# Kernel tuning notes

Measured on AMD Instinct MI355X. Metric: run time of the kernel, lower is better.

## Reference

```python
import jax, jax.numpy as jnp
import numpy as np

D_MODEL = 1024
NUM_HEADS = 16
D_K = D_MODEL // NUM_HEADS


def setup_inputs() -> dict:
    key = jax.random.key(0)
    ks = jax.random.split(key, 11)
    s = 1.0 / np.sqrt(D_MODEL)
    return {
        "Q": jax.random.normal(ks[0], (2, 2048, D_MODEL), jnp.float32),
        "K": jax.random.normal(ks[1], (2, 2048, D_MODEL), jnp.float32),
        "V": jax.random.normal(ks[2], (2, 2048, D_MODEL), jnp.float32),
        "W_Q": jax.random.uniform(ks[3], (D_MODEL, D_MODEL), jnp.float32, -s, s),
        "b_Q": jax.random.uniform(ks[4], (D_MODEL,), jnp.float32, -s, s),
        "W_K": jax.random.uniform(ks[5], (D_K, D_MODEL), jnp.float32, -s, s),
        "b_K": jax.random.uniform(ks[6], (D_K,), jnp.float32, -s, s),
        "W_V": jax.random.uniform(ks[7], (D_K, D_MODEL), jnp.float32, -s, s),
        "b_V": jax.random.uniform(ks[8], (D_K,), jnp.float32, -s, s),
        "W_O": jax.random.uniform(ks[9], (D_MODEL, D_MODEL), jnp.float32, -s, s),
        "b_O": jax.random.uniform(ks[10], (D_MODEL,), jnp.float32, -s, s),
    }


def reference(Q, K, V, W_Q, b_Q, W_K, b_K, W_V, b_V, W_O, b_O):
    B, S, _ = Q.shape
    # Q projection -> [B, H, S, d_k]
    q = (Q @ W_Q.T + b_Q).reshape(B, S, NUM_HEADS, D_K).transpose(0, 2, 1, 3)
    # shared single-head K/V -> [B, S, d_k] (broadcast across heads)
    k = K @ W_K.T + b_K
    v = V @ W_V.T + b_V
    scale = 1.0 / jnp.sqrt(jnp.asarray(D_K, q.dtype))
    scores = jnp.einsum('bhqd,bkd->bhqk', q, k) * scale  # [B,H,S,S]
    attn = jax.nn.softmax(scores, axis=-1)
    out = jnp.einsum('bhqk,bkd->bhqd', attn, v)  # [B,H,S,d_k]
    out = out.transpose(0, 2, 1, 3).reshape(B, S, D_MODEL)
    return out @ W_O.T + b_O
```

## Files before the change

kernel.cpp:

```cpp
#include <hip/hip_runtime.h>
#include <hip/hip_bf16.h>
#include <math.h>

#define D_MODEL 1024
#define NUM_HEADS 16
#define DK 64
#define BATCH 2
#define SEQ 2048
#define MROWS (BATCH * SEQ)

#define QSCALE (0.125f * 1.4426950408889634f)

typedef __attribute__((ext_vector_type(8))) short bf16x8;
typedef __attribute__((ext_vector_type(4))) float f32x4;

static __device__ __forceinline__ short f2bf(float f) {
    __hip_bfloat16 h = __float2bfloat16(f);
    union { __hip_bfloat16 h; short s; } c; c.h = h; return c.s;
}

static __device__ __forceinline__ unsigned pkbf2(float a, float b) {
    __hip_bfloat162 h = __float22bfloat162_rn(make_float2(a, b));
    union { __hip_bfloat162 h; unsigned u; } c; c.h = h; return c.u;
}

static __device__ __forceinline__ void gload16(const void* g, void* l) {
    __builtin_amdgcn_global_load_lds(
        (const __attribute__((address_space(1))) unsigned int*)g,
        (__attribute__((address_space(3))) unsigned int*)l, 16, 0, 0);
}

__global__ __launch_bounds__(256) void cvt6(
    const float* __restrict__ q, const float* __restrict__ k,
    const float* __restrict__ v, const float* __restrict__ wq,
    const float* __restrict__ wo, const float* __restrict__ wk,
    const float* __restrict__ wv,
    short* __restrict__ qo, short* __restrict__ ko, short* __restrict__ vo,
    short* __restrict__ wqo, short* __restrict__ woo, short* __restrict__ wko,
    short* __restrict__ wvo)
{
    const int NB = (MROWS * D_MODEL) / 8;
    const int NW = (D_MODEL * D_MODEL) / 8;
    const int NS = (DK * D_MODEL) / 8;
    const int total = 3 * NB + 2 * NW + 2 * NS;
    for (int g = blockIdx.x * 256 + threadIdx.x; g < total; g += gridDim.x * 256) {
        const float* s; short* d; int x = g;
        if (x < NB)            { s = q;  d = qo;  }
        else if ((x -= NB) < NB) { s = k;  d = ko;  }
        else if ((x -= NB) < NB) { s = v;  d = vo;  }
        else if ((x -= NB) < NW) { s = wq; d = wqo; }
        else if ((x -= NW) < NW) { s = wo; d = woo; }
        else if ((x -= NW) < NS) { s = wk; d = wko; }
        else                     { x -= NS; s = wv; d = wvo; }
        float4 a = ((const float4*)s)[x * 2];
        float4 b = ((const float4*)s)[x * 2 + 1];
        uint4 hv;
        hv.x = pkbf2(a.x, a.y); hv.y = pkbf2(a.z, a.w);
        hv.z = pkbf2(b.x, b.y); hv.w = pkbf2(b.z, b.w);
        ((uint4*)d)[x] = hv;
    }
}

template<int MODE, int BM, int BN>
__global__ __launch_bounds__(256) void gemm97(
    const short* __restrict__ A, const short* __restrict__ W,
    const float* __restrict__ bias, void* __restrict__ Cp,
    const short* __restrict__ A2, const short* __restrict__ W2,
    const float* __restrict__ bias2, void* __restrict__ Cp2,
    int M, int N, int K, float outmult)
{
    constexpr int MI = BM / 32;
    constexpr int NI = BN / 32;
    constexpr int ACH = BM / 32;
    constexpr int WCH = BN / 32;
    __shared__ short As[BM * 64];
    __shared__ short Ws[BN * 64];

    int sel = 0;
    if (MODE == 2) {
        sel = blockIdx.y;
        if (sel) { A = A2; W = W2; bias = bias2; Cp = Cp2; }
    }
    const int bm = blockIdx.x * BM;
    const int bn = (MODE == 2) ? 0 : blockIdx.y * BN;
    const int tid = threadIdx.x;
    const int l = tid & 63, w = tid >> 6;
    const int lr = l & 15, lg = l >> 4;
    const int wm = (w >> 1) * (BM / 2), wn = (w & 1) * (BN / 2);

    f32x4 acc[MI][NI];
    #pragma unroll
    for (int mi = 0; mi < MI; mi++)
        #pragma unroll
        for (int ni = 0; ni < NI; ni++)
            acc[mi][ni] = (f32x4){0.f, 0.f, 0.f, 0.f};

    const int srow = l >> 3;
    const int scol = (l & 7) * 8;

    for (int k0 = 0; k0 < K; k0 += 64) {
        __syncthreads();
        #pragma unroll
        for (int i = 0; i < ACH; i++) {
            int c = w * ACH + i;
            gload16(A + (size_t)(bm + 8 * c + srow) * K + k0 + scol, As + c * 512);
        }
        #pragma unroll
        for (int i = 0; i < WCH; i++) {
            int c = w * WCH + i;
            gload16(W + (size_t)(bn + 8 * c + srow) * K + k0 + scol, Ws + c * 512);
        }
        __syncthreads();
        #pragma unroll
        for (int ks = 0; ks < 2; ks++) {
            bf16x8 af[MI], bf[NI];
            #pragma unroll
            for (int mi = 0; mi < MI; mi++)
                af[mi] = *(const bf16x8*)&As[(wm + mi * 16 + lr) * 64 + ks * 32 + 8 * lg];
            #pragma unroll
            for (int ni = 0; ni < NI; ni++)
                bf[ni] = *(const bf16x8*)&Ws[(wn + ni * 16 + lr) * 64 + ks * 32 + 8 * lg];
            #pragma unroll
            for (int mi = 0; mi < MI; mi++)
                #pragma unroll
                for (int ni = 0; ni < NI; ni++)
                    acc[mi][ni] = __builtin_amdgcn_mfma_f32_16x16x32_bf16(
                        af[mi], bf[ni], acc[mi][ni], 0, 0, 0);
        }
    }

    #pragma unroll
    for (int ni = 0; ni < NI; ni++) {
        int col = bn + wn + ni * 16 + lr;
        float bv = bias[col];
        #pragma unroll
        for (int mi = 0; mi < MI; mi++) {
            #pragma unroll
            for (int r = 0; r < 4; r++) {
                int row = bm + wm + mi * 16 + lg * 4 + r;
                float val = (acc[mi][ni][r] + bv) * outmult;
                if (MODE == 0) {
                    ((short*)Cp)[(size_t)row * N + col] = f2bf(val);
                } else if (MODE == 1) {
                    ((float*)Cp)[(size_t)row * N + col] = val;
                } else {
                    if (sel == 0) {
                        ((short*)Cp)[(size_t)row * DK + col] = f2bf(val);
                    } else {
                        int bi = row >> 11, si = row & (SEQ - 1);
                        ((short*)Cp)[((size_t)bi * DK + col) * SEQ + si] = f2bf(val);
                    }
                }
            }
        }
    }
}

__global__ __launch_bounds__(256, 4) void mqa_attn_lds(
    const short* __restrict__ qb, const short* __restrict__ kb,
    const short* __restrict__ vt, short* __restrict__ ob)
{
    __shared__ char KsB[2][64 * 128];
    __shared__ char VsB[2][64 * 128];
    __shared__ char Ps[4][16 * 128];
    const int h = blockIdx.y, b = blockIdx.z;
    const int tid = threadIdx.x;
    const int l = tid & 63, w = tid >> 6;
    const int lr = l & 15, lg = l >> 4;
    const int q0 = blockIdx.x * 64 + w * 16;
    char* myPs = Ps[w];

    bf16x8 qf[2];
    #pragma unroll
    for (int kk = 0; kk < 2; kk++)
        qf[kk] = *(const bf16x8*)(
            qb + (size_t)(b * SEQ + q0 + lr) * D_MODEL + h * DK + kk * 32 + 8 * lg);

    int srow[2], scol[2];
    #pragma unroll
    for (int i = 0; i < 2; i++) {
        int s = i * 256 + w * 64 + l;
        srow[i] = s >> 3;
        int cb = (s & 7) * 16;
        scol[i] = (cb ^ ((srow[i] & 7) << 4)) >> 1;
    }

    f32x4 o[4];
    #pragma unroll
    for (int dt = 0; dt < 4; dt++)
        o[dt] = (f32x4){0.f, 0.f, 0.f, 0.f};
    float m_i = -1e30f;
    float l_l = 0.f;

    #pragma unroll
    for (int i = 0; i < 2; i++) {
        gload16(kb + (size_t)(b * SEQ + 0 + srow[i]) * DK + scol[i],
                KsB[0] + (i * 256 + w * 64) * 16);
        gload16(vt + (size_t)(b * DK + srow[i]) * SEQ + 0 + scol[i],
                VsB[0] + (i * 256 + w * 64) * 16);
    }

    for (int t = 0; t < SEQ / 64; t++) {
        const int cur = t & 1;
        const int kt = t * 64;
        __syncthreads();
        if (t + 1 < SEQ / 64) {
            const int ktn = kt + 64;
            #pragma unroll
            for (int i = 0; i < 2; i++) {
                gload16(kb + (size_t)(b * SEQ + ktn + srow[i]) * DK + scol[i],
                        KsB[cur ^ 1] + (i * 256 + w * 64) * 16);
                gload16(vt + (size_t)(b * DK + srow[i]) * SEQ + ktn + scol[i],
                        VsB[cur ^ 1] + (i * 256 + w * 64) * 16);
            }
        }
        const char* Kc = KsB[cur];
        const char* Vc = VsB[cur];

        f32x4 s[4];
        #pragma unroll
        for (int j = 0; j < 4; j++) s[j] = (f32x4){0.f, 0.f, 0.f, 0.f};
        #pragma unroll
        for (int kk = 0; kk < 2; kk++) {
            bf16x8 kf[4];
            #pragma unroll
            for (int j = 0; j < 4; j++) {
                int row = j * 16 + lr;
                kf[j] = *(const bf16x8*)(Kc + row * 128 + ((kk * 64 + 16 * lg) ^ ((row & 7) << 4)));
            }
            __builtin_amdgcn_s_setprio(1);
            #pragma unroll
            for (int j = 0; j < 4; j++)
                s[j] = __builtin_amdgcn_mfma_f32_16x16x32_bf16(
                    kf[j], qf[kk], s[j], 0, 0, 0);
            __builtin_amdgcn_s_setprio(0);
        }

        {
            float mA = fmaxf(fmaxf(s[0][0], s[0][1]), s[0][2]);
            float mB = fmaxf(fmaxf(s[0][3], s[1][0]), s[1][1]);
            float mC = fmaxf(fmaxf(s[1][2], s[1][3]), s[2][0]);
            float mD = fmaxf(fmaxf(s[2][1], s[2][2]), s[2][3]);
            float mE = fmaxf(fmaxf(s[3][0], s[3][1]), s[3][2]);
            float mx = fmaxf(fmaxf(fmaxf(mA, mB), mC),
                             fmaxf(fmaxf(mD, mE), s[3][3]));

            if (__any(mx > m_i + 8.0f)) {
                float mxf = fmaxf(mx, __shfl_xor(mx, 16));
                mxf = fmaxf(mxf, __shfl_xor(mxf, 32));
                float mn = fmaxf(m_i, mxf);
                float corr = __builtin_amdgcn_exp2f(m_i - mn);
                m_i = mn;
                l_l *= corr;
                #pragma unroll
                for (int dt = 0; dt < 4; dt++)
                    o[dt] *= corr;
            }
            const float mnv = m_i;

            float rs = 0.f;
            char* base = myPs + lr * 128;
            const int sw = (lr & 7) << 4;
            #pragma unroll
            for (int j = 0; j < 4; j++) {
                float p0 = __builtin_amdgcn_exp2f(s[j][0] - mnv);
                float p1 = __builtin_amdgcn_exp2f(s[j][1] - mnv);
                float p2 = __builtin_amdgcn_exp2f(s[j][2] - mnv);
                float p3 = __builtin_amdgcn_exp2f(s[j][3] - mnv);
                rs += (p0 + p1) + (p2 + p3);
                uint2 pk;
                pk.x = pkbf2(p0, p1);
                pk.y = pkbf2(p2, p3);
                *(uint2*)(base + ((j * 32 + lg * 8) ^ sw)) = pk;
            }
            l_l += rs;
        }

        #pragma unroll
        for (int kk = 0; kk < 2; kk++) {
            bf16x8 vf[4], pf;
            #pragma unroll
            for (int dt = 0; dt < 4; dt++) {
                int row = dt * 16 + lr;
                vf[dt] = *(const bf16x8*)(Vc + row * 128 + ((kk * 64 + 16 * lg) ^ ((row & 7) << 4)));
            }
            pf = *(bf16x8*)(myPs + lr * 128 + ((kk * 64 + 16 * lg) ^ ((lr & 7) << 4)));
            __builtin_amdgcn_s_setprio(1);
            #pragma unroll
            for (int dt = 0; dt < 4; dt++)
                o[dt] = __builtin_amdgcn_mfma_f32_16x16x32_bf16(
                    vf[dt], pf, o[dt], 0, 0, 0);
            __builtin_amdgcn_s_setprio(0);
        }
    }

    float lt = l_l;
    lt += __shfl_xor(lt, 16);
    lt += __shfl_xor(lt, 32);
    float inv = 1.0f / lt;
    size_t grow = (size_t)(b * SEQ + q0 + lr);
    #pragma unroll
    for (int dt = 0; dt < 4; dt++) {
        uint2 pk;
        pk.x = pkbf2(o[dt][0] * inv, o[dt][1] * inv);
        pk.y = pkbf2(o[dt][2] * inv, o[dt][3] * inv);
        *(uint2*)(ob + grow * D_MODEL + h * DK + dt * 16 + lg * 4) = pk;
    }
}

extern "C" void kernel_launch(void* const* d_in, const int* in_sizes, int n_in,
                              void* d_out, int out_size, void* d_ws, size_t ws_size,
                              hipStream_t stream) {
    const float* Q   = (const float*)d_in[0];
    const float* K   = (const float*)d_in[1];
    const float* V   = (const float*)d_in[2];
    const float* W_Q = (const float*)d_in[3];
    const float* b_Q = (const float*)d_in[4];
    const float* W_K = (const float*)d_in[5];
    const float* b_K = (const float*)d_in[6];
    const float* W_V = (const float*)d_in[7];
    const float* b_V = (const float*)d_in[8];
    const float* W_O = (const float*)d_in[9];
    const float* b_O = (const float*)d_in[10];
    float* out = (float*)d_out;

    short* Qb  = (short*)d_ws;
    short* Kb  = Qb  + (size_t)MROWS * D_MODEL;
    short* Vb  = Kb  + (size_t)MROWS * D_MODEL;
    short* WQb = Vb  + (size_t)MROWS * D_MODEL;
    short* WKb = WQb + (size_t)D_MODEL * D_MODEL;
    short* WVb = WKb + (size_t)DK * D_MODEL;
    short* WOb = WVb + (size_t)DK * D_MODEL;
    short* qb  = WOb + (size_t)D_MODEL * D_MODEL;
    short* kb  = qb  + (size_t)MROWS * D_MODEL;
    short* vt  = kb  + (size_t)MROWS * DK;
    short* aws = vt  + (size_t)MROWS * DK;

    cvt6<<<2048, 256, 0, stream>>>(Q, K, V, W_Q, W_O, W_K, W_V,
                                   Qb, Kb, Vb, WQb, WOb, WKb, WVb);

    gemm97<0, 64, 128><<<dim3(MROWS / 64, D_MODEL / 128), 256, 0, stream>>>(
        Qb, WQb, b_Q, qb, nullptr, nullptr, nullptr, nullptr,
        MROWS, D_MODEL, D_MODEL, QSCALE);
    gemm97<2, 64, 64><<<dim3(MROWS / 64, 2), 256, 0, stream>>>(
        Kb, WKb, b_K, kb, Vb, WVb, b_V, vt, MROWS, DK, D_MODEL, 1.0f);
    mqa_attn_lds<<<dim3(SEQ / 64, NUM_HEADS, BATCH), 256, 0, stream>>>(
        qb, kb, vt, aws);
    gemm97<1, 64, 128><<<dim3(MROWS / 64, D_MODEL / 128), 256, 0, stream>>>(
        aws, WOb, b_O, out, nullptr, nullptr, nullptr, nullptr,
        MROWS, D_MODEL, D_MODEL, 1.0f);
}
```

Measured before the change: 130.9 us.

## Keep softmax probabilities in registers by permuting V^T sequence layout

The V projection now writes V^T with the sequence index permuted inside each 64-key block, so the MFMA output layout of the S tile matches the B-operand layout the PV MFMA expects. Probabilities are packed straight into bf16x8 registers instead of going through a per-wave LDS staging buffer. This removes LDS writes and reads plus their latency each iteration, and drops the shared P buffer, which lowers LDS use. V fragments are also preloaded before the softmax, which raises register pressure.

Result: faster. 126.5 us (-3.4%).

```diff
diff --git a/kernel.cpp b/kernel.cpp
--- a/kernel.cpp
+++ b/kernel.cpp
@@ -148,7 +148,11 @@
                         ((short*)Cp)[(size_t)row * DK + col] = f2bf(val);
                     } else {
                         int bi = row >> 11, si = row & (SEQ - 1);
-                        ((short*)Cp)[((size_t)bi * DK + col) * SEQ + si] = f2bf(val);
+                        int s6 = si & 63;
+                        int sperm = (si & ~63) | (s6 & 32) |
+                                    (((s6 >> 3) & 1) << 4) | (((s6 >> 2) & 1) << 3) |
+                                    (((s6 >> 4) & 1) << 2) | (s6 & 3);
+                        ((short*)Cp)[((size_t)bi * DK + col) * SEQ + sperm] = f2bf(val);
                     }
                 }
             }
@@ -162,13 +166,11 @@
 {
     __shared__ char KsB[2][64 * 128];
     __shared__ char VsB[2][64 * 128];
-    __shared__ char Ps[4][16 * 128];
     const int h = blockIdx.y, b = blockIdx.z;
     const int tid = threadIdx.x;
     const int l = tid & 63, w = tid >> 6;
     const int lr = l & 15, lg = l >> 4;
     const int q0 = blockIdx.x * 64 + w * 16;
-    char* myPs = Ps[w];
 
     bf16x8 qf[2];
     #pragma unroll
@@ -236,6 +238,16 @@
             __builtin_amdgcn_s_setprio(0);
         }
 
+        bf16x8 vf[2][4];
+        #pragma unroll
+        for (int kk = 0; kk < 2; kk++)
+            #pragma unroll
+            for (int dt = 0; dt < 4; dt++) {
+                int row = dt * 16 + lr;
+                vf[kk][dt] = *(const bf16x8*)(Vc + row * 128 + ((kk * 64 + 16 * lg) ^ ((row & 7) << 4)));
+            }
+
+        union { unsigned u[4]; bf16x8 v; } pku[2];
         {
             float mA = fmaxf(fmaxf(s[0][0], s[0][1]), s[0][2]);
             float mB = fmaxf(fmaxf(s[0][3], s[1][0]), s[1][1]);
@@ -258,40 +270,36 @@
             }
             const float mnv = m_i;
 
+            float p[4][4];
             float rs = 0.f;
-            char* base = myPs + lr * 128;
-            const int sw = (lr & 7) << 4;
             #pragma unroll
             for (int j = 0; j < 4; j++) {
-                float p0 = __builtin_amdgcn_exp2f(s[j][0] - mnv);
-                float p1 = __builtin_amdgcn_exp2f(s[j][1] - mnv);
-                float p2 = __builtin_amdgcn_exp2f(s[j][2] - mnv);
-                float p3 = __builtin_amdgcn_exp2f(s[j][3] - mnv);
-                rs += (p0 + p1) + (p2 + p3);
-                uint2 pk;
-                pk.x = pkbf2(p0, p1);
-                pk.y = pkbf2(p2, p3);
-                *(uint2*)(base + ((j * 32 + lg * 8) ^ sw)) = pk;
+                p[j][0] = __builtin_amdgcn_exp2f(s[j][0] - mnv);
+                p[j][1] = __builtin_amdgcn_exp2f(s[j][1] - mnv);
+                p[j][2] = __builtin_amdgcn_exp2f(s[j][2] - mnv);
+                p[j][3] = __builtin_amdgcn_exp2f(s[j][3] - mnv);
+                rs += (p[j][0] + p[j][1]) + (p[j][2] + p[j][3]);
             }
             l_l += rs;
-        }
-
-        #pragma unroll
-        for (int kk = 0; kk < 2; kk++) {
-            bf16x8 vf[4], pf;
-            #pragma unroll
-            for (int dt = 0; dt < 4; dt++) {
-                int row = dt * 16 + lr;
-                vf[dt] = *(const bf16x8*)(Vc + row * 128 + ((kk * 64 + 16 * lg) ^ ((row & 7) << 4)));
-            }
-            pf = *(bf16x8*)(myPs + lr * 128 + ((kk * 64 + 16 * lg) ^ ((lr & 7) << 4)));
-            __builtin_amdgcn_s_setprio(1);
+
+            pku[0].u[0] = pkbf2(p[0][0], p[0][1]);
+            pku[0].u[1] = pkbf2(p[0][2], p[0][3]);
+            pku[0].u[2] = pkbf2(p[1][0], p[1][1]);
+            pku[0].u[3] = pkbf2(p[1][2], p[1][3]);
+            pku[1].u[0] = pkbf2(p[2][0], p[2][1]);
+            pku[1].u[1] = pkbf2(p[2][2], p[2][3]);
+            pku[1].u[2] = pkbf2(p[3][0], p[3][1]);
+            pku[1].u[3] = pkbf2(p[3][2], p[3][3]);
+        }
+
+        __builtin_amdgcn_s_setprio(1);
+        #pragma unroll
+        for (int kk = 0; kk < 2; kk++)
             #pragma unroll
             for (int dt = 0; dt < 4; dt++)
                 o[dt] = __builtin_amdgcn_mfma_f32_16x16x32_bf16(
-                    vf[dt], pf, o[dt], 0, 0, 0);
-            __builtin_amdgcn_s_setprio(0);
-        }
+                    vf[kk][dt], pku[kk].v, o[dt], 0, 0, 0);
+        __builtin_amdgcn_s_setprio(0);
     }
 
     float lt = l_l;
```
